# Optimization experiments

Measured on AMD Instinct MI355X. Metric: run time of the kernel, lower is better.

The kernel has to match this reference:

```python
import jax, jax.numpy as jnp
import numpy as np

B, C, H, W = 2, 128, 64, 96
RADIUS = (4, 4)
NLEVEL = 3
OUT_FEAT = 128
GN_GROUPS = OUT_FEAT // 16
EPS = 1e-5


def setup_inputs() -> dict:
    key = jax.random.key(0)
    k1, k2, k3, k4, k5 = jax.random.split(key, 5)
    fmap1 = jax.random.normal(k1, (B, C, H, W), dtype=jnp.float32)
    fmap2 = jax.random.normal(k2, (B, C, H, W), dtype=jnp.float32)
    # target coords in pixel units: channel 0 = x in [0, W-1], channel 1 = y in [0, H-1]
    scale = jnp.array([W - 1, H - 1], dtype=jnp.float32).reshape(1, 2, 1, 1)
    target_xy = jax.random.uniform(k3, (B, 2, H, W), dtype=jnp.float32) * scale
    in_ch = NLEVEL * (2 * RADIUS[0] + 1) * (2 * RADIUS[1] + 1)  # 243
    conv_w = jax.random.normal(k4, (OUT_FEAT, in_ch), dtype=jnp.float32) / np.float32(np.sqrt(in_ch))
    conv_b = jax.random.normal(k5, (OUT_FEAT,), dtype=jnp.float32) * 0.01
    gn_w = jnp.ones((OUT_FEAT,), dtype=jnp.float32)
    gn_b = jnp.zeros((OUT_FEAT,), dtype=jnp.float32)
    return {"fmap1": fmap1, "fmap2": fmap2, "target_xy": target_xy,
            "conv_w": conv_w, "conv_b": conv_b, "gn_w": gn_w, "gn_b": gn_b}


def _bilinear_lookup(corr_flat, H2, W2, x, y):
    """corr_flat: [B,H1,W1,H2*W2]; x,y: [B,H1,W1,K] pixel coords. Zero padding outside."""
    x0 = jnp.floor(x); y0 = jnp.floor(y)
    x1 = x0 + 1.0; y1 = y0 + 1.0
    wx1 = x - x0; wx0 = 1.0 - wx1
    wy1 = y - y0; wy0 = 1.0 - wy1

    def gather(xi, yi):
        valid = (xi >= 0) & (xi <= W2 - 1) & (yi >= 0) & (yi <= H2 - 1)
        xc = jnp.clip(xi, 0, W2 - 1).astype(jnp.int32)
        yc = jnp.clip(yi, 0, H2 - 1).astype(jnp.int32)
        v = jnp.take_along_axis(corr_flat, yc * W2 + xc, axis=3)
        return jnp.where(valid, v, jnp.float32(0.0))

    return (gather(x0, y0) * wx0 * wy0 + gather(x1, y0) * wx1 * wy0 +
            gather(x0, y1) * wx0 * wy1 + gather(x1, y1) * wx1 * wy1)


def _forward(fmap1, fmap2, target_xy, conv_w, conv_b, gn_w, gn_b):
    b, c, h1, w1 = fmap1.shape
    # all-pairs correlation: [B,H1,W1,H1,W1]
    corr = jnp.einsum('bcij,bckl->bijkl', fmap1, fmap2) / jnp.sqrt(jnp.float32(c))
    # window offsets, torch ordering: row index -> dy, col index -> dx, row-major flatten
    dy, dx = jnp.meshgrid(jnp.arange(-RADIUS[0], RADIUS[0] + 1, dtype=jnp.float32),
                          jnp.arange(-RADIUS[1], RADIUS[1] + 1, dtype=jnp.float32),
                          indexing='ij')
    dy = dy.reshape(-1); dx = dx.reshape(-1)  # [K]

    out_corr = []
    corr_l = corr
    for i in range(NLEVEL):
        if i > 0:
            H2p, W2p = corr_l.shape[3], corr_l.shape[4]
            corr_l = corr_l.reshape(b, h1, w1, H2p // 2, 2, W2p // 2, 2).mean(axis=(4, 6))
        H2, W2 = corr_l.shape[3], corr_l.shape[4]
        corr_flat = corr_l.reshape(b, h1, w1, H2 * W2)
        inv = jnp.float32(1.0 / (2 ** i))
        x = target_xy[:, 0, :, :, None] * inv + dx[None, None, None, :]  # [B,H1,W1,K]
        y = target_xy[:, 1, :, :, None] * inv + dy[None, None, None, :]
        inter = _bilinear_lookup(corr_flat, H2, W2, x, y)  # [B,H1,W1,K]
        out_corr.append(jnp.transpose(inter, (0, 3, 1, 2)))  # [B,K,H1,W1]
    feat = jnp.concatenate(out_corr, axis=1)  # [B, NLEVEL*K, H1, W1]

    # 1x1 conv + GroupNorm + LeakyReLU(0.1)
    y_ = jnp.einsum('bchw,oc->bohw', feat, conv_w) + conv_b[None, :, None, None]
    g = GN_GROUPS
    yr = y_.reshape(b, g, OUT_FEAT // g, h1, w1)
    mean = yr.mean(axis=(2, 3, 4), keepdims=True)
    var = yr.var(axis=(2, 3, 4), keepdims=True)
    yn = ((yr - mean) * jax.lax.rsqrt(var + EPS)).reshape(b, OUT_FEAT, h1, w1)
    yn = yn * gn_w[None, :, None, None] + gn_b[None, :, None, None]
    return jnp.where(yn > 0, yn, 0.1 * yn)


def reference(fmap1, fmap2, target_xy, conv_w, conv_b, gn_w, gn_b):
    return _forward(fmap1, fmap2, target_xy, conv_w, conv_b, gn_w, gn_b)
```

## Files before the change

### kernel.cpp

```cpp
#include <hip/hip_runtime.h>

#define HW   6144
#define WID  96
#define HEI  64
#define IC   243

#define HF1   0u
#define HL0   1572864u
#define HL1   3145728u
#define HL2   3538944u
#define WTH   3637248u
#define FYP   1835008u
#define FPART 3407872u
#define FST2  3432448u

typedef _Float16 v2h __attribute__((ext_vector_type(2)));
typedef _Float16 h8  __attribute__((ext_vector_type(8)));
typedef float f32x4 __attribute__((ext_vector_type(4)));

#if __has_builtin(__builtin_amdgcn_fdot2)
#define FDOT2(a,b,c) __builtin_amdgcn_fdot2((a),(b),(c),false)
#else
static __device__ __forceinline__ float fdot2_fb(v2h a, v2h b, float c){
    return c + (float)a[0]*(float)b[0] + (float)a[1]*(float)b[1];
}
#define FDOT2(a,b,c) fdot2_fb((a),(b),(c))
#endif

static __device__ __forceinline__ v2h g2(h8 v, int i){ v2h r; r[0]=v[2*i]; r[1]=v[2*i+1]; return r; }

template<int CTRL>
static __device__ __forceinline__ float dppadd(float x) {
    int t = __builtin_amdgcn_update_dpp(0, __builtin_bit_cast(int, x), CTRL, 0xf, 0xf, false);
    return x + __builtin_bit_cast(float, t);
}

__global__ void k_t(const float* __restrict__ f1, const float* __restrict__ f2,
                    float* __restrict__ ws) {
    _Float16* wh = (_Float16*)ws;
    const float* src = blockIdx.z ? f2 : f1;
    _Float16* dst = wh + (blockIdx.z ? HL0 : HF1);
    const int t = threadIdx.x;
    const int pix0 = blockIdx.x * 64;
    const int c0 = blockIdx.y * 32;
    const int b = pix0 / HW;
    const int pb = pix0 - b * HW;
    __shared__ float sT[32][65];
    const int px = t & 63;
    const int cb8 = (t >> 6) * 8;
    #pragma unroll
    for (int i = 0; i < 8; i++)
        sT[cb8 + i][px] = src[((size_t)(b * 128 + c0 + cb8 + i)) * HW + pb + px];
    __syncthreads();
    const int pw = t >> 2;
    const int cg = (t & 3) * 8;
    h8 hv;
    #pragma unroll
    for (int i = 0; i < 8; i++) hv[i] = (_Float16)sT[cg + i][pw];
    *(h8*)(dst + ((size_t)(pix0 + pw)) * 128 + c0 + cg) = hv;
}

__global__ void k_wt(const float* __restrict__ w, float* __restrict__ ws) {
    _Float16* wth = (_Float16*)ws + WTH;
    int tid = blockIdx.x * 256 + threadIdx.x;
    int o = tid >> 8, k = tid & 255;
    wth[tid] = (k < IC) ? (_Float16)w[o * IC + k] : (_Float16)0.f;
}

__global__ void k_pool(const _Float16* __restrict__ src, _Float16* __restrict__ dst,
                       int Ho, int Wo) {
    int gt = blockIdx.x * 256 + threadIdx.x;
    int oc = gt & 15;
    int rest = gt >> 4;
    int x = rest % Wo; rest /= Wo;
    int y = rest % Ho; int b = rest / Ho;
    int Wi = Wo * 2;
    const _Float16* s = src + ((size_t)((b * (Ho * 2) + 2 * y) * Wi + 2 * x)) * 128 + oc * 8;
    h8 a  = *(const h8*)s;
    h8 bb = *(const h8*)(s + 128);
    h8 c  = *(const h8*)(s + (size_t)Wi * 128);
    h8 d  = *(const h8*)(s + (size_t)Wi * 128 + 128);
    h8 r;
    #pragma unroll
    for (int j = 0; j < 8; j++)
        r[j] = (_Float16)(0.25f * ((float)a[j] + (float)bb[j] + (float)c[j] + (float)d[j]));
    *(h8*)(dst + (size_t)gt * 8) = r;
}

__launch_bounds__(256)
__global__ void k_corr_conv(const float* __restrict__ txy, const float* __restrict__ cb,
                            float* __restrict__ ws) {
    const _Float16* wh = (const _Float16*)ws;
    const int tid = threadIdx.x;
    const int j = blockIdx.x;
    const int xcd = j & 7;
    const int slot = j >> 3;
    const int b = xcd >> 2;
    const int pblk = slot * 4 + (xcd & 3);
    const int pb0 = pblk * 8;
    const int pix0 = b * HW + pb0;

    __shared__ _Float16 sGh[8 * 300];
    __shared__ _Float16 sFh[8 * 256];
    __shared__ float sLev[8 * 12];

    if (tid < 24) {
        int p = tid / 3, lev = tid - 3 * p;
        float tx = txy[(b * 2 + 0) * HW + pb0 + p];
        float ty = txy[(b * 2 + 1) * HW + pb0 + p];
        float inv = (lev == 0) ? 1.f : ((lev == 1) ? 0.5f : 0.25f);
        float xs = tx * inv, ys = ty * inv;
        float X0 = floorf(xs), Y0 = floorf(ys);
        sLev[p * 12 + lev * 4 + 0] = X0;
        sLev[p * 12 + lev * 4 + 1] = Y0;
        sLev[p * 12 + lev * 4 + 2] = xs - X0;
        sLev[p * 12 + lev * 4 + 3] = ys - Y0;
    }
    if (tid < 104) {
        int p = tid / 13, k = 243 + tid - (tid / 13) * 13;
        int kb = k >> 3, ke = k & 7;
        sFh[p * 256 + ((kb ^ (p & 7)) << 3) + ke] = (_Float16)0.f;
    }

    const int l = tid & 7;
    const int grp8 = tid >> 3;
    const int p = grp8 >> 2;
    const int rs = grp8 & 3;
    const _Float16* f1p = wh + HF1 + ((size_t)(pix0 + p)) * 128 + l * 8;
    const h8 av0 = *(const h8*)(f1p);
    const h8 av1 = *(const h8*)(f1p + 64);

    __syncthreads();

    const float scale = 0.08838834764831845f;
    for (int it = 0; it < 8; ++it) {
        int flat = rs + it * 4;
        bool rowok = (flat < 30);
        int fl = rowok ? flat : 0;
        int lev = (fl >= 20) ? 2 : ((fl >= 10) ? 1 : 0);
        int row = fl - lev * 10;
        const int WL = WID >> lev, HL = HEI >> lev;
        const _Float16* f2b = wh + ((lev == 0) ? HL0 : ((lev == 1) ? HL1 : HL2))
                              + (size_t)b * HL * WL * 128;
        const int X0 = (int)sLev[p * 12 + lev * 4 + 0];
        const int Y0 = (int)sLev[p * 12 + lev * 4 + 1];
        int y = Y0 - 4 + row;
        bool yok = rowok && ((unsigned)y < (unsigned)HL);
        int yc = min(max(y, 0), HL - 1);
        const _Float16* rowp = f2b + (size_t)(yc * WL) * 128 + l * 8;
        _Float16* sGp = sGh + p * 300 + lev * 100 + row * 10;
        #pragma unroll
        for (int c4 = 0; c4 < 10; ++c4) {
            int x = X0 - 4 + c4;
            bool ok = yok && ((unsigned)x < (unsigned)WL);
            int xc = min(max(x, 0), WL - 1);
            const _Float16* colp = rowp + xc * 128;
            h8 bv0 = *(const h8*)(colp);
            h8 bv1 = *(const h8*)(colp + 64);
            float d = FDOT2(g2(av0, 0), g2(bv0, 0), 0.f);
            d = FDOT2(g2(av0, 1), g2(bv0, 1), d);
            d = FDOT2(g2(av0, 2), g2(bv0, 2), d);
            d = FDOT2(g2(av0, 3), g2(bv0, 3), d);
            d = FDOT2(g2(av1, 0), g2(bv1, 0), d);
            d = FDOT2(g2(av1, 1), g2(bv1, 1), d);
            d = FDOT2(g2(av1, 2), g2(bv1, 2), d);
            d = FDOT2(g2(av1, 3), g2(bv1, 3), d);
            d = dppadd<0xB1>(d);
            d = dppadd<0x4E>(d);
            d = dppadd<0x141>(d);
            if (l == 0 && rowok) sGp[c4] = ok ? (_Float16)(d * scale) : (_Float16)0.f;
        }
    }
    __syncthreads();

    for (int idx = tid; idx < 8 * IC; idx += 256) {
        int k = idx >> 3, p2 = idx & 7;
        int lev = (k < 81) ? 0 : ((k < 162) ? 1 : 2);
        int kk = k - lev * 81;
        int dyi = (kk * 57) >> 9, dxi = kk - 9 * dyi;
        float fx = sLev[p2 * 12 + lev * 4 + 2];
        float fy = sLev[p2 * 12 + lev * 4 + 3];
        const _Float16* Gp = sGh + p2 * 300 + lev * 100 + dyi * 10 + dxi;
        float v = (1.f - fy) * ((1.f - fx) * (float)Gp[0] + fx * (float)Gp[1])
                +        fy  * ((1.f - fx) * (float)Gp[10] + fx * (float)Gp[11]);
        int kb = k >> 3, ke = k & 7;
        sFh[p2 * 256 + ((kb ^ (p2 & 7)) << 3) + ke] = (_Float16)v;
    }
    __syncthreads();

    const int lane = tid & 63;
    const int wv = __builtin_amdgcn_readfirstlane(tid >> 6);
    const int pc = lane & 15;
    const int kq = lane >> 4;
    const _Float16* wth = wh + WTH;
    const int om0 = wv, om1 = wv + 4;
    const _Float16* wtb0 = wth + (om0 * 16 + pc) * 256 + kq * 8;
    const _Float16* wtb1 = wth + (om1 * 16 + pc) * 256 + kq * 8;
    f32x4 acc0 = {0.f, 0.f, 0.f, 0.f}, acc1 = {0.f, 0.f, 0.f, 0.f};
    const int pcl = pc & 7;
    #pragma unroll
    for (int s = 0; s < 8; ++s) {
        int kb = s * 4 + kq;
        h8 bvv = *(const h8*)(sFh + pcl * 256 + ((kb ^ (pcl & 7)) << 3));
        h8 a0 = *(const h8*)(wtb0 + s * 32);
        h8 a1 = *(const h8*)(wtb1 + s * 32);
        acc0 = __builtin_amdgcn_mfma_f32_16x16x32_f16(a0, bvv, acc0, 0, 0, 0);
        acc1 = __builtin_amdgcn_mfma_f32_16x16x32_f16(a1, bvv, acc1, 0, 0, 0);
    }
    const int row4 = kq * 4;
    float4 bb0 = *(const float4*)&cb[om0 * 16 + row4];
    float4 bb1 = *(const float4*)&cb[om1 * 16 + row4];
    float y00 = acc0[0] + bb0.x, y01 = acc0[1] + bb0.y, y02 = acc0[2] + bb0.z, y03 = acc0[3] + bb0.w;
    float y10 = acc1[0] + bb1.x, y11 = acc1[1] + bb1.y, y12 = acc1[2] + bb1.z, y13 = acc1[3] + bb1.w;
    if (pc < 8) {
        float* op0 = ws + FYP + ((size_t)(pix0 + pc)) * 128 + om0 * 16 + row4;
        float* op1 = ws + FYP + ((size_t)(pix0 + pc)) * 128 + om1 * 16 + row4;
        op0[0] = y00; op0[1] = y01; op0[2] = y02; op0[3] = y03;
        op1[0] = y10; op1[1] = y11; op1[2] = y12; op1[3] = y13;
    }
    bool val = (pc < 8);
    float s0 = val ? (y00 + y01 + y02 + y03) : 0.f;
    float q0 = val ? (y00*y00 + y01*y01 + y02*y02 + y03*y03) : 0.f;
    float s1 = val ? (y10 + y11 + y12 + y13) : 0.f;
    float q1 = val ? (y10*y10 + y11*y11 + y12*y12 + y13*y13) : 0.f;
    #pragma unroll
    for (int m = 1; m < 64; m <<= 1) {
        s0 += __shfl_xor(s0, m);
        q0 += __shfl_xor(q0, m);
        s1 += __shfl_xor(s1, m);
        q1 += __shfl_xor(q1, m);
    }
    if (lane == 0) {
        float* pp = ws + FPART + (size_t)(b * 768 + pblk) * 16;
        pp[om0 * 2]     = s0;
        pp[om0 * 2 + 1] = q0;
        pp[om1 * 2]     = s1;
        pp[om1 * 2 + 1] = q1;
    }
}

__global__ void k_gnred(float* __restrict__ ws) {
    const int bg = blockIdx.x;
    const int b = bg >> 3, om = bg & 7;
    const int t = threadIdx.x;
    float s = 0.f, q = 0.f;
    for (int blk = b * 768 + t; blk < (b + 1) * 768; blk += 256) {
        const float* pp = ws + FPART + (size_t)blk * 16 + om * 2;
        s += pp[0]; q += pp[1];
    }
    __shared__ float rs[256], rq[256];
    rs[t] = s; rq[t] = q;
    __syncthreads();
    for (int st = 128; st > 0; st >>= 1) {
        if (t < st) { rs[t] += rs[t + st]; rq[t] += rq[t + st]; }
        __syncthreads();
    }
    if (t == 0) {
        const float invN = 1.f / (float)(HW * 16);
        float mean = rs[0] * invN;
        float var = rq[0] * invN - mean * mean;
        ws[FST2 + bg * 2]     = mean;
        ws[FST2 + bg * 2 + 1] = rsqrtf(var + 1e-5f);
    }
}

__global__ void k_finish(const float* __restrict__ gw, const float* __restrict__ gb,
                         const float* __restrict__ ws, float* __restrict__ out) {
    const int t = threadIdx.x;
    const int pix0 = blockIdx.x * 64;
    const int b = pix0 / HW;
    const int pb = pix0 - b * HW;
    __shared__ float sO[128][65];
    __shared__ float sM[8], sR[8];
    if (t < 8) {
        sM[t] = ws[FST2 + (b * 8 + t) * 2];
        sR[t] = ws[FST2 + (b * 8 + t) * 2 + 1];
    }
    __syncthreads();
    #pragma unroll
    for (int it = 0; it < 32; ++it) {
        int idx = it * 256 + t;
        int px = idx >> 7, c = idx & 127;
        float v = ws[FYP + ((size_t)(pix0 + px)) * 128 + c];
        int g = c >> 4;
        v = (v - sM[g]) * sR[g] * gw[c] + gb[c];
        sO[c][px] = v > 0.f ? v : 0.1f * v;
    }
    __syncthreads();
    #pragma unroll
    for (int it = 0; it < 32; ++it) {
        int idx = it * 256 + t;
        int px = idx & 63, c = idx >> 6;
        out[((size_t)(b * 128 + c)) * HW + pb + px] = sO[c][px];
    }
}

extern "C" void kernel_launch(void* const* d_in, const int* in_sizes, int n_in,
                              void* d_out, int out_size, void* d_ws, size_t ws_size,
                              hipStream_t stream) {
    const float* f1  = (const float*)d_in[0];
    const float* f2  = (const float*)d_in[1];
    const float* txy = (const float*)d_in[2];
    const float* cw  = (const float*)d_in[3];
    const float* cb  = (const float*)d_in[4];
    const float* gw  = (const float*)d_in[5];
    const float* gb  = (const float*)d_in[6];
    float* ws = (float*)d_ws;
    _Float16* whp = (_Float16*)d_ws;
    float* out = (float*)d_out;

    k_t<<<dim3(192, 4, 2), 256, 0, stream>>>(f1, f2, ws);
    k_wt<<<128, 256, 0, stream>>>(cw, ws);
    k_pool<<<192, 256, 0, stream>>>(whp + HL0, whp + HL1, 32, 48);
    k_pool<<<48, 256, 0, stream>>>(whp + HL1, whp + HL2, 16, 24);
    k_corr_conv<<<1536, 256, 0, stream>>>(txy, cb, ws);
    k_gnred<<<16, 256, 0, stream>>>(ws);
    k_finish<<<192, 256, 0, stream>>>(gw, gb, ws, out);
}
```

Baseline: 79.18 us.

## Precompute level-2 correlation table with MFMA and gather windows from it

Adds a kernel that computes the full level-2 correlation (each pixel against all 384 coarse cells) with 16x16x32 f16 MFMA instructions and stores it as an fp16 table in the workspace. The main correlation kernel then drops level 2 from its per-pixel dot-product loop, going from 8 iterations to 5. Level-2 window values are now gathered from the table. This moves scattered dot products to matrix cores, in exchange for an extra launch and a table of roughly 9.4 MB in fp16 that must be written and read back.

Measured after the change: 83.37 us. 5.3% more time.

```diff
diff --git a/kernel.cpp b/kernel.cpp
--- a/kernel.cpp
+++ b/kernel.cpp
@@ -13,6 +13,7 @@
 #define FYP   1835008u
 #define FPART 3407872u
 #define FST2  3432448u
+#define T2H   6864960u
 
 typedef _Float16 v2h __attribute__((ext_vector_type(2)));
 typedef _Float16 h8  __attribute__((ext_vector_type(8)));
@@ -88,6 +89,45 @@
 }
 
 __launch_bounds__(256)
+__global__ void k_tab2(float* __restrict__ ws) {
+    const _Float16* wh = (const _Float16*)ws;
+    _Float16* t2 = (_Float16*)ws + T2H;
+    const int b = blockIdx.y;
+    const int pix0 = blockIdx.x * 16;
+    const int lane = threadIdx.x & 63;
+    const int wv = __builtin_amdgcn_readfirstlane(threadIdx.x >> 6);
+    const int p = lane & 15;
+    const int kq = lane >> 4;
+    const size_t pixg = (size_t)(b * HW + pix0 + p);
+    const _Float16* f1p = wh + HF1 + pixg * 128 + kq * 8;
+    const h8 bf0 = *(const h8*)(f1p);
+    const h8 bf1 = *(const h8*)(f1p + 32);
+    const h8 bf2 = *(const h8*)(f1p + 64);
+    const h8 bf3 = *(const h8*)(f1p + 96);
+    const _Float16* f2b = wh + HL2 + (size_t)b * 384 * 128;
+    const float scale = 0.08838834764831845f;
+    #pragma unroll
+    for (int pass = 0; pass < 6; ++pass) {
+        int cell0 = pass * 64 + wv * 16;
+        const _Float16* ap = f2b + ((size_t)(cell0 + p)) * 128 + kq * 8;
+        h8 a0 = *(const h8*)(ap);
+        h8 a1 = *(const h8*)(ap + 32);
+        h8 a2 = *(const h8*)(ap + 64);
+        h8 a3 = *(const h8*)(ap + 96);
+        f32x4 acc = {0.f, 0.f, 0.f, 0.f};
+        acc = __builtin_amdgcn_mfma_f32_16x16x32_f16(a0, bf0, acc, 0, 0, 0);
+        acc = __builtin_amdgcn_mfma_f32_16x16x32_f16(a1, bf1, acc, 0, 0, 0);
+        acc = __builtin_amdgcn_mfma_f32_16x16x32_f16(a2, bf2, acc, 0, 0, 0);
+        acc = __builtin_amdgcn_mfma_f32_16x16x32_f16(a3, bf3, acc, 0, 0, 0);
+        _Float16* op = t2 + pixg * 384 + cell0 + kq * 4;
+        op[0] = (_Float16)(acc[0] * scale);
+        op[1] = (_Float16)(acc[1] * scale);
+        op[2] = (_Float16)(acc[2] * scale);
+        op[3] = (_Float16)(acc[3] * scale);
+    }
+}
+
+__launch_bounds__(256)
 __global__ void k_corr_conv(const float* __restrict__ txy, const float* __restrict__ cb,
                             float* __restrict__ ws) {
     const _Float16* wh = (const _Float16*)ws;
@@ -133,19 +173,17 @@
     __syncthreads();
 
     const float scale = 0.08838834764831845f;
-    for (int it = 0; it < 8; ++it) {
-        int flat = rs + it * 4;
-        bool rowok = (flat < 30);
-        int fl = rowok ? flat : 0;
-        int lev = (fl >= 20) ? 2 : ((fl >= 10) ? 1 : 0);
+    for (int it = 0; it < 5; ++it) {
+        int fl = rs + it * 4;
+        int lev = (fl >= 10) ? 1 : 0;
         int row = fl - lev * 10;
         const int WL = WID >> lev, HL = HEI >> lev;
-        const _Float16* f2b = wh + ((lev == 0) ? HL0 : ((lev == 1) ? HL1 : HL2))
+        const _Float16* f2b = wh + ((lev == 0) ? HL0 : HL1)
                               + (size_t)b * HL * WL * 128;
         const int X0 = (int)sLev[p * 12 + lev * 4 + 0];
         const int Y0 = (int)sLev[p * 12 + lev * 4 + 1];
         int y = Y0 - 4 + row;
-        bool yok = rowok && ((unsigned)y < (unsigned)HL);
+        bool yok = (unsigned)y < (unsigned)HL;
         int yc = min(max(y, 0), HL - 1);
         const _Float16* rowp = f2b + (size_t)(yc * WL) * 128 + l * 8;
         _Float16* sGp = sGh + p * 300 + lev * 100 + row * 10;
@@ -168,7 +206,22 @@
             d = dppadd<0xB1>(d);
             d = dppadd<0x4E>(d);
             d = dppadd<0x141>(d);
-            if (l == 0 && rowok) sGp[c4] = ok ? (_Float16)(d * scale) : (_Float16)0.f;
+            if (l == 0) sGp[c4] = ok ? (_Float16)(d * scale) : (_Float16)0.f;
+        }
+    }
+    {
+        const _Float16* t2 = wh + T2H;
+        for (int idx = tid; idx < 800; idx += 256) {
+            int pp = idx / 100;
+            int rem = idx - pp * 100;
+            int rr = rem / 10, cc = rem - rr * 10;
+            int X0 = (int)sLev[pp * 12 + 2 * 4 + 0];
+            int Y0 = (int)sLev[pp * 12 + 2 * 4 + 1];
+            int y = Y0 - 4 + rr, x = X0 - 4 + cc;
+            bool ok = ((unsigned)x < 24u) && ((unsigned)y < 16u);
+            int xc = min(max(x, 0), 23), yc = min(max(y, 0), 15);
+            _Float16 v = t2[((size_t)(pix0 + pp)) * 384 + yc * 24 + xc];
+            sGh[pp * 300 + 200 + rr * 10 + cc] = ok ? v : (_Float16)0.f;
         }
     }
     __syncthreads();
@@ -313,6 +366,7 @@
     k_wt<<<128, 256, 0, stream>>>(cw, ws);
     k_pool<<<192, 256, 0, stream>>>(whp + HL0, whp + HL1, 32, 48);
     k_pool<<<48, 256, 0, stream>>>(whp + HL1, whp + HL2, 16, 24);
+    k_tab2<<<dim3(384, 2), 256, 0, stream>>>(ws);
     k_corr_conv<<<1536, 256, 0, stream>>>(txy, cb, ws);
     k_gnred<<<16, 256, 0, stream>>>(ws);
     k_finish<<<192, 256, 0, stream>>>(gw, gb, ws, out);
```
